# Kernel optimization log

Measured on AMD Instinct MI355X. Metric: run time of the kernel, lower is better.

## Reference

```python
import jax, jax.numpy as jnp
import numpy as np

IN_DIM = 40
EMB = 20
HID = 20
T = 400000


def setup_inputs() -> dict:
    key = jax.random.key(0)
    ks = jax.random.split(key, 12)
    s_in = 1.0 / np.sqrt(IN_DIM)
    s_h = 1.0 / np.sqrt(HID)
    u = lambda k, shape, s: jax.random.uniform(k, shape, jnp.float32, -s, s)
    return {
        "in_states": jax.random.normal(ks[0], (T, IN_DIM), jnp.float32),
        "W_inp": u(ks[1], (EMB, IN_DIM), s_in),
        "b_inp": u(ks[2], (EMB,), s_in),
        "W_ih0": u(ks[3], (4 * HID, EMB), s_h),
        "W_hh0": u(ks[4], (4 * HID, HID), s_h),
        "b_ih0": u(ks[5], (4 * HID,), s_h),
        "b_hh0": u(ks[6], (4 * HID,), s_h),
        "W_ih1": u(ks[7], (4 * HID, HID), s_h),
        "W_hh1": u(ks[8], (4 * HID, HID), s_h),
        "b_ih1": u(ks[9], (4 * HID,), s_h),
        "b_hh1": u(ks[10], (4 * HID,), s_h),
        "W_out": u(ks[11], (1, HID), s_h),
        "b_out": jnp.zeros((1,), jnp.float32),
    }


def _lstm_cell(gates, h_prev, c_prev, W_hh):
    # PyTorch gate order: i, f, g, o
    g = gates + h_prev @ W_hh.T  # [4H]
    i = jax.nn.sigmoid(g[0 * HID:1 * HID])
    f = jax.nn.sigmoid(g[1 * HID:2 * HID])
    gg = jnp.tanh(g[2 * HID:3 * HID])
    o = jax.nn.sigmoid(g[3 * HID:4 * HID])
    c = f * c_prev + i * gg
    h = o * jnp.tanh(c)
    return h, c


def reference(in_states, W_inp, b_inp, W_ih0, W_hh0, b_ih0, b_hh0,
              W_ih1, W_hh1, b_ih1, b_hh1, W_out, b_out):
    # input projection for the whole sequence (big memory-bound GEMV batch)
    x = in_states @ W_inp.T + b_inp                       # [T, EMB]
    pre0 = x @ W_ih0.T + (b_ih0 + b_hh0)                  # [T, 4H]
    bias1 = b_ih1 + b_hh1

    def step(carry, pre0_t):
        h0, c0, h1, c1 = carry
        h0, c0 = _lstm_cell(pre0_t, h0, c0, W_hh0)
        gates1 = h0 @ W_ih1.T + bias1
        h1, c1 = _lstm_cell(gates1, h1, c1, W_hh1)
        return (h0, c0, h1, c1), h1

    z = jnp.zeros((HID,), in_states.dtype)
    (h0, c0, h1, c1), hs = jax.lax.scan(step, (z, z, z, z), pre0)
    outputs = (hs @ W_out.T + b_out).reshape(T, 1, 1)     # [T, 1, 1]
    h_n = jnp.stack([h0, h1])[:, None, :]                 # [2, 1, HID]
    c_n = jnp.stack([c0, c1])[:, None, :]
    return outputs, h_n, c_n
```

## Files before the change

### kernel.cpp

```cpp
#include <hip/hip_runtime.h>
#include <hip/hip_fp16.h>

#define T_LEN   400000
#define IN_DIM  40
#define EMB     20
#define HID     20
#define G4      80

#define CHUNK_L 64
#define NCHUNK  6250
#define NBLK    3125
#define WARM    48
#define WARMB   (WARM / 8)
#define NBATCH  ((CHUNK_L + WARM) / 8)

#define PRE0_TW 160
#define SD_STR  168
#define SLOT_H  (G4 * 8)

#define PRE0_BYTE_OFF 32768

typedef _Float16 h2v __attribute__((ext_vector_type(2)));
typedef _Float16 h8v __attribute__((ext_vector_type(8)));
typedef float f32x4 __attribute__((ext_vector_type(4)));

#if __has_builtin(__builtin_amdgcn_fdot2)
#define FDOT2(a, b, c) __builtin_amdgcn_fdot2((a), (b), (c), false)
#else
#define FDOT2(a, b, c) ((float)(a)[0] * (float)(b)[0] + (float)(a)[1] * (float)(b)[1] + (c))
#endif

#if __has_builtin(__builtin_amdgcn_exp2f)
#define EXP2F(x) __builtin_amdgcn_exp2f(x)
#else
#define EXP2F(x) exp2f(x)
#endif
#if __has_builtin(__builtin_amdgcn_rcpf)
#define RCPF(x) __builtin_amdgcn_rcpf(x)
#else
#define RCPF(x) (1.0f / (x))
#endif

__device__ __forceinline__ float actg(float x, float c, float a, float b) {
  float e = EXP2F(c * x);
  float r = RCPF(1.f + e);
  return fmaf(a, r, b);
}
#define TANH_C (-2.885390082f)
#define SIGM_C (-1.442695041f)

#define WSYNC() do { __builtin_amdgcn_wave_barrier(); asm volatile("" ::: "memory"); } while (0)

__device__ __forceinline__ int orig_row(int r) { return (r & 3) * 20 + (r >> 2); }

__device__ __forceinline__ void loadrow_h(h2v* dst, const float* p) {
#pragma unroll
  for (int k = 0; k < 10; ++k) {
    h2v v; v[0] = (_Float16)p[2 * k]; v[1] = (_Float16)p[2 * k + 1];
    dst[k] = v;
  }
}

__device__ __forceinline__ void load10h(h2v* dst, const _Float16* base) {
  const uint4* p4 = (const uint4*)base;
  uint4 q0 = p4[0], q1 = p4[1];
  uint2 q2 = *(const uint2*)(base + 16);
  unsigned u[10] = {q0.x, q0.y, q0.z, q0.w, q1.x, q1.y, q1.z, q1.w, q2.x, q2.y};
#pragma unroll
  for (int k = 0; k < 10; ++k) dst[k] = __builtin_bit_cast(h2v, u[k]);
}

__device__ __forceinline__ h8v packh8(const float4& a, const float4& b) {
  __half2 p0 = __halves2half2(__float2half(a.x), __float2half(a.y));
  __half2 p1 = __halves2half2(__float2half(a.z), __float2half(a.w));
  __half2 p2 = __halves2half2(__float2half(b.x), __float2half(b.y));
  __half2 p3 = __halves2half2(__float2half(b.z), __float2half(b.w));
  uint4 u = make_uint4(*(unsigned*)&p0, *(unsigned*)&p1, *(unsigned*)&p2, *(unsigned*)&p3);
  return __builtin_bit_cast(h8v, u);
}

__global__ void prep_kernel(const float* __restrict__ W_inp, const float* __restrict__ b_inp,
                            const float* __restrict__ W_ih0, const float* __restrict__ b_ih0,
                            const float* __restrict__ b_hh0, const float* __restrict__ b_ih1,
                            const float* __restrict__ b_hh1, const float* __restrict__ W_out,
                            float* __restrict__ ws) {
  int tid = threadIdx.x;
  for (int idx = tid; idx < G4 * IN_DIM; idx += 256) {
    int r = idx / IN_DIM, j = idx % IN_DIM;
    int o = orig_row(r);
    float s = 0.f;
#pragma unroll
    for (int k = 0; k < EMB; ++k) s += W_ih0[o * EMB + k] * W_inp[k * IN_DIM + j];
    ws[idx] = s;
  }
  if (tid < G4) {
    int o = orig_row(tid);
    float s = b_ih0[o] + b_hh0[o];
#pragma unroll
    for (int k = 0; k < EMB; ++k) s += W_ih0[o * EMB + k] * b_inp[k];
    ws[3200 + tid] = s;
    ws[3280 + tid] = b_ih1[o] + b_hh1[o];
  }
  if (tid < 10) {
    __half2 p = __halves2half2(__float2half(W_out[2 * tid]), __float2half(W_out[2 * tid + 1]));
    ((unsigned*)ws)[3360 + tid] = *(unsigned*)&p;
  }
  __syncthreads();
  for (int i = tid; i < 2560; i += 256) {
    int r = i >> 5, kp = i & 31;
    unsigned v = 0;
    if (kp < 20) {
      __half2 p = __halves2half2(__float2half(ws[r * IN_DIM + 2 * kp]),
                                 __float2half(ws[r * IN_DIM + 2 * kp + 1]));
      v = *(unsigned*)&p;
    }
    ((unsigned*)ws)[5552 + i] = v;
  }
}

__global__ __launch_bounds__(128) void pre0_kernel(const float* __restrict__ in_states,
                                                   const float* __restrict__ ws,
                                                   __half* __restrict__ pre0b) {
  __shared__ __align__(16) _Float16 sD[80 * SD_STR];
  const int tid = threadIdx.x;
  const int l  = tid & 63;
  const int w  = tid >> 6;
  const int rb = l & 15;
  const int kg = l >> 4;
  const int t0 = blockIdx.x * PRE0_TW;
  const int tw = 80 * w;

  h8v afr[5][2];
  {
    const unsigned* wp = (const unsigned*)ws + 5552;
#pragma unroll
    for (int m = 0; m < 5; ++m)
#pragma unroll
      for (int ki = 0; ki < 2; ++ki) {
        uint4 q = *(const uint4*)&wp[(16 * m + rb) * 32 + 16 * ki + kg * 4];
        afr[m][ki] = __builtin_bit_cast(h8v, q);
      }
  }
  float4 bias4[5];
#pragma unroll
  for (int m = 0; m < 5; ++m) bias4[m] = *(const float4*)&ws[3200 + 16 * m + kg * 4];

#pragma unroll
  for (int n = 0; n < 5; ++n) {
    const int t = t0 + tw + 16 * n + rb;
    const float* xr = in_states + (size_t)t * IN_DIM;
    float4 x0 = *(const float4*)(xr + kg * 8);
    float4 x1 = *(const float4*)(xr + kg * 8 + 4);
    float4 y0 = make_float4(0.f, 0.f, 0.f, 0.f), y1 = y0;
    if (kg == 0) { y0 = *(const float4*)(xr + 32); y1 = *(const float4*)(xr + 36); }
    h8v b0 = packh8(x0, x1);
    h8v b1 = packh8(y0, y1);

    f32x4 acc[5];
#pragma unroll
    for (int m = 0; m < 5; ++m) {
      acc[m][0] = bias4[m].x; acc[m][1] = bias4[m].y;
      acc[m][2] = bias4[m].z; acc[m][3] = bias4[m].w;
    }
#pragma unroll
    for (int m = 0; m < 5; ++m) {
      acc[m] = __builtin_amdgcn_mfma_f32_16x16x32_f16(afr[m][0], b0, acc[m], 0, 0, 0);
      acc[m] = __builtin_amdgcn_mfma_f32_16x16x32_f16(afr[m][1], b1, acc[m], 0, 0, 0);
    }
#pragma unroll
    for (int m = 0; m < 5; ++m)
#pragma unroll
      for (int r = 0; r < 4; ++r)
        sD[(16 * m + kg * 4 + r) * SD_STR + tw + 16 * n + rb] = (_Float16)acc[m][r];
  }
  __syncthreads();

  for (int i = tid; i < (PRE0_TW / 8) * 80; i += 128) {
    int q   = i / 80;
    int row = i % 80;
    size_t t8 = (size_t)blockIdx.x * (PRE0_TW / 8) + q;
    uint4 v = *(const uint4*)&sD[row * SD_STR + q * 8];
    *(uint4*)(pre0b + t8 * SLOT_H + row * 8) = v;
  }
}

__global__ __launch_bounds__(64, 2) void scan_kernel(
    const __half* __restrict__ pre0b, const float* __restrict__ ws,
    const float* __restrict__ W_hh0, const float* __restrict__ W_ih1,
    const float* __restrict__ W_hh1, const float* __restrict__ W_out,
    const float* __restrict__ b_out, float* __restrict__ out) {
  __shared__ __align__(16) float gp0s[2][96];
  __shared__ __align__(16) float r1ss[2][96];
  __shared__ __align__(16) float trashs[2][32];
  __shared__ __align__(16) _Float16 h0ss[2][32];
  __shared__ __align__(16) _Float16 h1ss[2][32];

  const int lane = threadIdx.x;
  const int l    = lane & 31;
  const int grp  = lane >> 5;
  const bool lo16 = (l < 16);

  const int chunk = blockIdx.x * 2 + grp;
  const int t0 = chunk * CHUNK_L - WARM;

  float* gp0 = gp0s[grp];
  float* r1s = r1ss[grp];
  _Float16* h0sg = h0ss[grp];
  _Float16* h1sg = h1ss[grp];

  h2v wG0a[10], wG0b[10], wR1a[10], wR1b[10], wS5[10], wI1a[10], wI1b[10], wS5c[10];
  loadrow_h(wG0a, W_hh0 + orig_row(l) * HID);
  loadrow_h(wG0b, W_hh0 + orig_row(l + 32) * HID);
  loadrow_h(wR1a, W_hh1 + orig_row(l) * HID);
  loadrow_h(wR1b, W_hh1 + orig_row(l + 32) * HID);
  loadrow_h(wS5, lo16 ? (W_hh0 + orig_row(64 + l) * HID)
                      : (W_hh1 + orig_row(64 + (l - 16)) * HID));
  loadrow_h(wI1a, W_ih1 + orig_row(l) * HID);
  loadrow_h(wI1b, W_ih1 + orig_row(l + 32) * HID);
  loadrow_h(wS5c, W_ih1 + orig_row(lo16 ? l : (64 + (l - 16))) * HID);
  h2v wouth[10];
  {
    const unsigned* woutp = (const unsigned*)ws + 3360;
#pragma unroll
    for (int k = 0; k < 10; ++k) wouth[k] = __builtin_bit_cast(h2v, woutp[k]);
  }
  const float b1a = ws[3280 + l];
  const float b1b = ws[3280 + l + 32];
  const float b1c = ws[3280 + 64 + (l & 15)];
  const float bout = b_out[0];

  const bool isT = ((l & 3) == 2);
  const float actC = isT ? TANH_C : SIGM_C;
  const float actA = isT ? 2.f : 1.f;
  const float actB = isT ? -1.f : 0.f;

  float* wr0 = &gp0[l];
  float* wr1 = &gp0[l + 32];
  float* wr4 = lo16 ? &gp0[64 + l] : &trashs[grp][l - 16];
  float* wc0 = &r1s[l];
  float* wc1 = &r1s[l + 32];
  float* wc4 = lo16 ? &trashs[grp][l] : &r1s[64 + (l - 16)];

  h2v hp0[10], hp1[10];
  {
    h2v z; z[0] = (_Float16)0.f; z[1] = (_Float16)0.f;
#pragma unroll
    for (int k = 0; k < 10; ++k) { hp0[k] = z; hp1[k] = z; }
  }
  float c0 = 0.f, c1 = 0.f, h0v = 0.f, h1v = 0.f;

  const int rowOffA = l * 8;
  const int rowOffB = (l + 32) * 8;
  const int rowOffC = (lo16 ? (64 + l) : (l + 32)) * 8;
#define SBASE(b) ((size_t)(((long)chunk * 8 - 6 + (b)) < 0 ? 0 : ((long)chunk * 8 - 6 + (b))) * SLOT_H)

  size_t base0 = SBASE(0);
  uint4 ua = *(const uint4*)(pre0b + base0 + rowOffA);
  uint4 ub = *(const uint4*)(pre0b + base0 + rowOffB);
  uint4 uc = *(const uint4*)(pre0b + base0 + rowOffC);

  for (int b = 0; b < NBATCH; ++b) {
    const int tb = t0 + 8 * b;
    const int bn = (b + 1 < NBATCH) ? b + 1 : b;
    const size_t nbase = SBASE(bn);
    uint4 na  = *(const uint4*)(pre0b + nbase + rowOffA);
    uint4 nb4 = *(const uint4*)(pre0b + nbase + rowOffB);
    uint4 nc4 = *(const uint4*)(pre0b + nbase + rowOffC);
    const bool upd = (tb >= 0);
    const bool live = (b >= WARMB);

#pragma unroll
    for (int s = 0; s < 8; ++s) {
      const float p_a = __half2float(((const __half*)&ua)[s]);
      const float p_b = __half2float(((const __half*)&ub)[s]);
      const float p_c = __half2float(((const __half*)&uc)[s]);

      float a0 = p_a, a1 = p_b;
      float r0 = b1a, r1v = b1b;
      float a4 = lo16 ? p_c : b1c;
#pragma unroll
      for (int k = 0; k < 10; ++k) {
        h2v hm = lo16 ? hp0[k] : hp1[k];
        a0  = FDOT2(wG0a[k], hp0[k], a0);
        a1  = FDOT2(wG0b[k], hp0[k], a1);
        r0  = FDOT2(wR1a[k], hp1[k], r0);
        r1v = FDOT2(wR1b[k], hp1[k], r1v);
        a4  = FDOT2(wS5[k],  hm, a4);
      }
      *wr0 = actg(a0, actC, actA, actB);
      *wr1 = actg(a1, actC, actA, actB);
      *wr4 = actg(a4, actC, actA, actB);
      WSYNC();

      if (l < 20) {
        float4 gv = ((const float4*)gp0)[l];
        float cn = fmaf(gv.y, c0, gv.x * gv.z);
        c0 = upd ? cn : c0;
        float tc = actg(c0, TANH_C, 2.f, -1.f);
        h0v = upd ? gv.w * tc : 0.f;
        h0sg[l] = (_Float16)h0v;
      }
      WSYNC();
      load10h(hp0, h0sg);

      float f0 = r0, f1 = r1v, f4 = a4;
#pragma unroll
      for (int k = 0; k < 10; ++k) {
        f0 = FDOT2(wI1a[k], hp0[k], f0);
        f1 = FDOT2(wI1b[k], hp0[k], f1);
        f4 = FDOT2(wS5c[k], hp0[k], f4);
      }
      *wc0 = actg(f0, actC, actA, actB);
      *wc1 = actg(f1, actC, actA, actB);
      *wc4 = actg(f4, actC, actA, actB);
      WSYNC();

      if (l < 20) {
        float4 gv = ((const float4*)r1s)[l];
        float cn = fmaf(gv.y, c1, gv.x * gv.z);
        c1 = upd ? cn : c1;
        float tc = actg(c1, TANH_C, 2.f, -1.f);
        h1v = upd ? gv.w * tc : 0.f;
        h1sg[l] = (_Float16)h1v;
      }
      WSYNC();
      load10h(hp1, h1sg);

      if (live) {
        float ov = bout;
#pragma unroll
        for (int k = 0; k < 10; ++k) ov = FDOT2(wouth[k], hp1[k], ov);
        if (l == 0) out[tb + s] = ov;
      }
    }
    ua = na; ub = nb4; uc = nc4;
  }

  if (blockIdx.x == NBLK - 1 && grp == 1 && l < 20) {
    out[T_LEN + l]      = h0v;
    out[T_LEN + 20 + l] = h1v;
    out[T_LEN + 40 + l] = c0;
    out[T_LEN + 60 + l] = c1;
  }
#undef SBASE
}

extern "C" void kernel_launch(void* const* d_in, const int* in_sizes, int n_in,
                              void* d_out, int out_size, void* d_ws, size_t ws_size,
                              hipStream_t stream) {
  const float* in_states = (const float*)d_in[0];
  const float* W_inp = (const float*)d_in[1];
  const float* b_inp = (const float*)d_in[2];
  const float* W_ih0 = (const float*)d_in[3];
  const float* W_hh0 = (const float*)d_in[4];
  const float* b_ih0 = (const float*)d_in[5];
  const float* b_hh0 = (const float*)d_in[6];
  const float* W_ih1 = (const float*)d_in[7];
  const float* W_hh1 = (const float*)d_in[8];
  const float* b_ih1 = (const float*)d_in[9];
  const float* b_hh1 = (const float*)d_in[10];
  const float* W_out = (const float*)d_in[11];
  const float* b_out = (const float*)d_in[12];

  float* ws = (float*)d_ws;
  __half* pre0b = (__half*)((char*)d_ws + PRE0_BYTE_OFF);
  float* outp = (float*)d_out;

  prep_kernel<<<1, 256, 0, stream>>>(W_inp, b_inp, W_ih0, b_ih0, b_hh0, b_ih1, b_hh1, W_out, ws);
  pre0_kernel<<<T_LEN / PRE0_TW, 128, 0, stream>>>(in_states, ws, pre0b);
  scan_kernel<<<NBLK, 64, 0, stream>>>(pre0b, ws, W_hh0, W_ih1, W_hh1, W_out, b_out, outp);
}
```

Measured before the change: 291.1 us.

## Compute LSTM cell update in-register via DPP quad broadcast and lengthen chunks

Replaces the LDS round-trip for gate activations (write gates to shared memory, barrier, 20 lanes read float4 and update the cell) with DPP quad broadcasts, so every quad computes its own cell update in registers and writes only h to shared memory. This removes one wave barrier and the shared-memory traffic per layer per timestep. Chunk length also goes from 64 to 80, which lowers the fraction of redundant warm-up steps but gives fewer blocks. The change adds redundant cell math on the lanes of each quad and relies on the interleaved gate row order lining up with quad lanes.

```diff
diff --git a/kernel.cpp b/kernel.cpp
--- a/kernel.cpp
+++ b/kernel.cpp
@@ -7,9 +7,9 @@
 #define HID     20
 #define G4      80
 
-#define CHUNK_L 64
-#define NCHUNK  6250
-#define NBLK    3125
+#define CHUNK_L 80
+#define NCHUNK  5000
+#define NBLK    2500
 #define WARM    48
 #define WARMB   (WARM / 8)
 #define NBATCH  ((CHUNK_L + WARM) / 8)
@@ -50,6 +50,20 @@
 #define SIGM_C (-1.442695041f)
 
 #define WSYNC() do { __builtin_amdgcn_wave_barrier(); asm volatile("" ::: "memory"); } while (0)
+
+#define QBC(v, ctrl) __builtin_bit_cast(float, __builtin_amdgcn_mov_dpp( \
+    __builtin_bit_cast(int, (v)), (ctrl), 0xF, 0xF, true))
+
+__device__ __forceinline__ void quad_cell(float gact, float& c, float& h, bool upd) {
+  float gi = QBC(gact, 0x00);
+  float gf = QBC(gact, 0x55);
+  float gg = QBC(gact, 0xAA);
+  float go = QBC(gact, 0xFF);
+  float cn = fmaf(gf, c, gi * gg);
+  c = upd ? cn : c;
+  float tc = actg(c, TANH_C, 2.f, -1.f);
+  h = upd ? go * tc : 0.f;
+}
 
 __device__ __forceinline__ int orig_row(int r) { return (r & 3) * 20 + (r >> 2); }
 
@@ -189,11 +203,9 @@
     const float* __restrict__ W_hh0, const float* __restrict__ W_ih1,
     const float* __restrict__ W_hh1, const float* __restrict__ W_out,
     const float* __restrict__ b_out, float* __restrict__ out) {
-  __shared__ __align__(16) float gp0s[2][96];
-  __shared__ __align__(16) float r1ss[2][96];
-  __shared__ __align__(16) float trashs[2][32];
   __shared__ __align__(16) _Float16 h0ss[2][32];
   __shared__ __align__(16) _Float16 h1ss[2][32];
+  __shared__ __align__(16) _Float16 t16s[2][32];
 
   const int lane = threadIdx.x;
   const int l    = lane & 31;
@@ -203,10 +215,9 @@
   const int chunk = blockIdx.x * 2 + grp;
   const int t0 = chunk * CHUNK_L - WARM;
 
-  float* gp0 = gp0s[grp];
-  float* r1s = r1ss[grp];
   _Float16* h0sg = h0ss[grp];
   _Float16* h1sg = h1ss[grp];
+  _Float16* t16  = t16s[grp];
 
   h2v wG0a[10], wG0b[10], wR1a[10], wR1b[10], wS5[10], wI1a[10], wI1b[10], wS5c[10];
   loadrow_h(wG0a, W_hh0 + orig_row(l) * HID);
@@ -234,12 +245,12 @@
   const float actA = isT ? 2.f : 1.f;
   const float actB = isT ? -1.f : 0.f;
 
-  float* wr0 = &gp0[l];
-  float* wr1 = &gp0[l + 32];
-  float* wr4 = lo16 ? &gp0[64 + l] : &trashs[grp][l - 16];
-  float* wc0 = &r1s[l];
-  float* wc1 = &r1s[l + 32];
-  float* wc4 = lo16 ? &trashs[grp][l] : &r1s[64 + (l - 16)];
+  _Float16* ph0a = ((l & 3) == 0) ? &h0sg[l >> 2]              : &t16[l];
+  _Float16* ph0b = ((l & 3) == 1) ? &h0sg[8 + (l >> 2)]        : &t16[l];
+  _Float16* ph0c = (lo16 && (l & 3) == 2) ? &h0sg[16 + (l >> 2)] : &t16[l];
+  _Float16* ph1a = ((l & 3) == 0) ? &h1sg[l >> 2]              : &t16[l];
+  _Float16* ph1b = ((l & 3) == 1) ? &h1sg[8 + (l >> 2)]        : &t16[l];
+  _Float16* ph1c = (!lo16 && (l & 3) == 2) ? &h1sg[16 + ((l - 16) >> 2)] : &t16[l];
 
   h2v hp0[10], hp1[10];
   {
@@ -247,12 +258,13 @@
 #pragma unroll
     for (int k = 0; k < 10; ++k) { hp0[k] = z; hp1[k] = z; }
   }
-  float c0 = 0.f, c1 = 0.f, h0v = 0.f, h1v = 0.f;
+  float c0a = 0.f, c0b = 0.f, c0c = 0.f, c1a = 0.f, c1b = 0.f, c1c = 0.f;
+  float h0a = 0.f, h0b = 0.f, h0c = 0.f, h1a = 0.f, h1b = 0.f, h1c = 0.f;
 
   const int rowOffA = l * 8;
   const int rowOffB = (l + 32) * 8;
   const int rowOffC = (lo16 ? (64 + l) : (l + 32)) * 8;
-#define SBASE(b) ((size_t)(((long)chunk * 8 - 6 + (b)) < 0 ? 0 : ((long)chunk * 8 - 6 + (b))) * SLOT_H)
+#define SBASE(b) ((size_t)(((long)chunk * 10 - 6 + (b)) < 0 ? 0 : ((long)chunk * 10 - 6 + (b))) * SLOT_H)
 
   size_t base0 = SBASE(0);
   uint4 ua = *(const uint4*)(pre0b + base0 + rowOffA);
@@ -287,19 +299,15 @@
         r1v = FDOT2(wR1b[k], hp1[k], r1v);
         a4  = FDOT2(wS5[k],  hm, a4);
       }
-      *wr0 = actg(a0, actC, actA, actB);
-      *wr1 = actg(a1, actC, actA, actB);
-      *wr4 = actg(a4, actC, actA, actB);
-      WSYNC();
-
-      if (l < 20) {
-        float4 gv = ((const float4*)gp0)[l];
-        float cn = fmaf(gv.y, c0, gv.x * gv.z);
-        c0 = upd ? cn : c0;
-        float tc = actg(c0, TANH_C, 2.f, -1.f);
-        h0v = upd ? gv.w * tc : 0.f;
-        h0sg[l] = (_Float16)h0v;
-      }
+      float ga0 = actg(a0, actC, actA, actB);
+      float ga1 = actg(a1, actC, actA, actB);
+      float ga4 = actg(a4, actC, actA, actB);
+      quad_cell(ga0, c0a, h0a, upd);
+      quad_cell(ga1, c0b, h0b, upd);
+      quad_cell(ga4, c0c, h0c, upd);
+      *ph0a = (_Float16)h0a;
+      *ph0b = (_Float16)h0b;
+      *ph0c = (_Float16)h0c;
       WSYNC();
       load10h(hp0, h0sg);
 
@@ -310,19 +318,15 @@
         f1 = FDOT2(wI1b[k], hp0[k], f1);
         f4 = FDOT2(wS5c[k], hp0[k], f4);
       }
-      *wc0 = actg(f0, actC, actA, actB);
-      *wc1 = actg(f1, actC, actA, actB);
-      *wc4 = actg(f4, actC, actA, actB);
-      WSYNC();
-
-      if (l < 20) {
-        float4 gv = ((const float4*)r1s)[l];
-        float cn = fmaf(gv.y, c1, gv.x * gv.z);
-        c1 = upd ? cn : c1;
-        float tc = actg(c1, TANH_C, 2.f, -1.f);
-        h1v = upd ? gv.w * tc : 0.f;
-        h1sg[l] = (_Float16)h1v;
-      }
+      float gf0 = actg(f0, actC, actA, actB);
+      float gf1 = actg(f1, actC, actA, actB);
+      float gf4 = actg(f4, actC, actA, actB);
+      quad_cell(gf0, c1a, h1a, upd);
+      quad_cell(gf1, c1b, h1b, upd);
+      quad_cell(gf4, c1c, h1c, upd);
+      *ph1a = (_Float16)h1a;
+      *ph1b = (_Float16)h1b;
+      *ph1c = (_Float16)h1c;
       WSYNC();
       load10h(hp1, h1sg);
 
@@ -336,11 +340,18 @@
     ua = na; ub = nb4; uc = nc4;
   }
 
-  if (blockIdx.x == NBLK - 1 && grp == 1 && l < 20) {
-    out[T_LEN + l]      = h0v;
-    out[T_LEN + 20 + l] = h1v;
-    out[T_LEN + 40 + l] = c0;
-    out[T_LEN + 60 + l] = c1;
+  if (blockIdx.x == NBLK - 1 && grp == 1 && (l & 3) == 0) {
+    const int u = l >> 2;
+    out[T_LEN + u]       = h0a;  out[T_LEN + 8 + u]  = h0b;
+    out[T_LEN + 20 + u]  = h1a;  out[T_LEN + 28 + u] = h1b;
+    out[T_LEN + 40 + u]  = c0a;  out[T_LEN + 48 + u] = c0b;
+    out[T_LEN + 60 + u]  = c1a;  out[T_LEN + 68 + u] = c1b;
+    if (lo16) {
+      out[T_LEN + 16 + u] = h0c;  out[T_LEN + 56 + u] = c0c;
+    } else {
+      const int u2 = (l - 16) >> 2;
+      out[T_LEN + 36 + u2] = h1c; out[T_LEN + 76 + u2] = c1c;
+    }
   }
 #undef SBASE
 }
```

Measured after the change: 319.9 us. 9.9% more time.
